# Optimization experiments

Hardware: AMD Instinct MI355X
Metric: run time of the kernel (lower is better)

Reference implementation:

```python
import jax, jax.numpy as jnp
import numpy as np

B, C, H, HEADS, WS, TOPK = 16, 112, 64, 4, 4, 128
NWH = H // WS          # 16 windows per side
NWIN = NWH * NWH       # 256 windows
HD = C // HEADS        # 28
SCALE = HD ** -0.5


def _topk_indices():
    # Geometric top-K closest full-res pixels per window center (level 0 of focal attention).
    f = H // NWH  # window stride on full-res grid
    qh = np.arange(NWH) * f + f // 2
    cq = np.stack(np.meshgrid(qh, qh, indexing='ij'), 0).reshape(2, -1)            # (2, NWIN)
    ck = np.stack(np.meshgrid(np.arange(H), np.arange(H), indexing='ij'), 0).reshape(2, -1)  # (2, H*H)
    d = np.sqrt(((cq[:, :, None].astype(np.float32) - ck[:, None, :]) ** 2).sum(0))
    return np.argsort(d, axis=1, kind='stable')[:, :TOPK].astype(np.int32)        # (NWIN, TOPK)


def setup_inputs() -> dict:
    key = jax.random.key(0)
    k1, k2, k3 = jax.random.split(key, 3)
    return {
        'x': jax.random.normal(k1, (B, C, H, H), jnp.float32),
        'Wqkv': jax.random.normal(k2, (3 * C, C), jnp.float32) * 0.02,
        'Wproj': jax.random.normal(k3, (C, C), jnp.float32) * 0.02,
        'bproj': jnp.zeros((C,), jnp.float32),
        'topk_idx': jnp.asarray(_topk_indices()),
    }


def reference(x, Wqkv, Wproj, bproj, topk_idx):
    Bv, Cv, Hv, Wv = x.shape
    nwin = (Hv // WS) * (Wv // WS)
    xt = jnp.transpose(x, (0, 2, 3, 1))                       # (B, H, W, C)
    qkv = jnp.einsum('bhwc,dc->bhwd', xt, Wqkv)               # 1x1 conv == matmul
    q, k, v = jnp.split(qkv, 3, axis=-1)
    # Window-partition queries: (B*nwin, heads, ws^2, hd)
    qw = q.reshape(Bv, Hv // WS, WS, Wv // WS, WS, Cv)
    qw = jnp.transpose(qw, (0, 1, 3, 2, 4, 5)).reshape(Bv * nwin, WS * WS, HEADS, HD)
    qw = jnp.transpose(qw, (0, 2, 1, 3)) * SCALE
    # Gather top-K K/V tokens per window from the full-resolution token list
    kf = k.reshape(Bv, Hv * Wv, HEADS, HD)
    vf = v.reshape(Bv, Hv * Wv, HEADS, HD)
    ksel = kf[:, topk_idx]                                    # (B, nwin, TOPK, heads, hd)
    vsel = vf[:, topk_idx]
    ksel = jnp.transpose(ksel, (0, 1, 3, 2, 4)).reshape(Bv * nwin, HEADS, TOPK, HD)
    vsel = jnp.transpose(vsel, (0, 1, 3, 2, 4)).reshape(Bv * nwin, HEADS, TOPK, HD)
    # Windowed attention over gathered KV
    attn = jax.nn.softmax(jnp.einsum('whqd,whkd->whqk', qw, ksel), axis=-1)
    o = jnp.einsum('whqk,whkd->whqd', attn, vsel)             # (B*nwin, heads, ws^2, hd)
    o = jnp.transpose(o, (0, 2, 1, 3)).reshape(Bv * nwin, WS * WS, Cv)
    # Window reverse -> (B, H, W, C)
    o = o.reshape(Bv, Hv // WS, Wv // WS, WS, WS, Cv)
    o = jnp.transpose(o, (0, 1, 3, 2, 4, 5)).reshape(Bv, Hv, Wv, Cv)
    out = jnp.einsum('bhwc,dc->bhwd', o, Wproj) + bproj
    return jnp.transpose(out, (0, 3, 1, 2))                   # (B, C, H, W)
```

## Files before the change

### kernel.cpp

```cpp
#include <hip/hip_runtime.h>
#include <hip/hip_bf16.h>
#include <cstdint>

#define B_ 16
#define C_ 112
#define HEADS_ 4
#define HD_ 28
#define NWIN_ 256
#define TOPK_ 128
#define D3_ 336
#define SCALE_ 0.18898223650461363f

typedef __attribute__((ext_vector_type(4))) float f32x4;
typedef __attribute__((ext_vector_type(8))) short short8;
typedef unsigned uint4u __attribute__((ext_vector_type(4), aligned(4)));

union Frag { unsigned u[4]; uint4 u4; short8 s; };

__device__ inline unsigned cvtpk(float a, float b) {
    unsigned r;
    asm("v_cvt_pk_bf16_f32 %0, %1, %2" : "=v"(r) : "v"(a), "v"(b));
    return r;
}
__device__ inline float bflo(unsigned u) { return __uint_as_float(u << 16); }
__device__ inline float bfhi(unsigned u) { return __uint_as_float(u & 0xFFFF0000u); }

__global__ __launch_bounds__(256) void wt_kernel(const float* __restrict__ W, const float* __restrict__ Wp,
                                                 uint4* __restrict__ WAq,
                                                 uint4* __restrict__ WAh, uint4* __restrict__ WAl) {
    const int id = blockIdx.x * 256 + threadIdx.x;
    if (id < 5376) {
        const int ks = id / 1344, rem = id % 1344;
        const int tile = rem >> 6, l = rem & 63;
        const int d = tile * 16 + (l & 15);
        const int cb = ks * 32 + (l >> 4) * 8;
        float v[8];
        #pragma unroll
        for (int j = 0; j < 8; ++j) { int c = cb + j; v[j] = (c < C_) ? W[d * C_ + c] : 0.f; }
        uint4 o;
        o.x = cvtpk(v[0], v[1]); o.y = cvtpk(v[2], v[3]);
        o.z = cvtpk(v[4], v[5]); o.w = cvtpk(v[6], v[7]);
        WAq[id] = o;
    } else if (id < 5376 + 1792) {
        const int id2 = id - 5376;
        const int ks = id2 / 448, rem = id2 % 448;
        const int tile = rem >> 6, l = rem & 63;
        const int d = tile * 16 + (l & 15);
        const int cb = ks * 32 + (l >> 4) * 8;
        float v[8];
        #pragma unroll
        for (int j = 0; j < 8; ++j) { int c = cb + j; v[j] = (c < C_) ? Wp[d * C_ + c] : 0.f; }
        unsigned hw_[4], lw_[4];
        #pragma unroll
        for (int p = 0; p < 4; ++p) {
            unsigned hh = cvtpk(v[2 * p], v[2 * p + 1]);
            hw_[p] = hh;
            lw_[p] = cvtpk(v[2 * p] - bflo(hh), v[2 * p + 1] - bfhi(hh));
        }
        WAh[id2] = make_uint4(hw_[0], hw_[1], hw_[2], hw_[3]);
        WAl[id2] = make_uint4(lw_[0], lw_[1], lw_[2], lw_[3]);
    }
}

__global__ __launch_bounds__(256) void qkv_kernel(const float* __restrict__ x,
                                                  const uint4* __restrict__ WAq,
                                                  ushort* __restrict__ qkv) {
    __shared__ unsigned xs[64][132];
    const int hw0 = blockIdx.x << 7;
    const int dblk = blockIdx.y;
    const int b = blockIdx.z;
    const int tid = threadIdx.x;
    for (int i = tid; i < 2048; i += 256) {
        const int c2 = i >> 5, j4 = (i & 31) << 2;
        uint4 o = make_uint4(0, 0, 0, 0);
        if (c2 < 56) {
            const float* r0 = x + (((size_t)b * C_ + 2 * c2) << 12) + hw0 + j4;
            float4 a = *(const float4*)r0;
            float4 c = *(const float4*)(r0 + 4096);
            o.x = cvtpk(a.x, c.x); o.y = cvtpk(a.y, c.y);
            o.z = cvtpk(a.z, c.z); o.w = cvtpk(a.w, c.w);
        }
        *(uint4*)&xs[c2][j4] = o;
    }
    __syncthreads();
    const int wv = tid >> 6, l = tid & 63, lq = l & 15, g = l >> 4;
    const int hwl = wv << 5;
    f32x4 acc[7][2] = {};
    #pragma unroll
    for (int ks = 0; ks < 4; ++ks) {
        Frag bf[2];
        #pragma unroll
        for (int n = 0; n < 2; ++n) {
            const int col = hwl + (n << 4) + lq;
            const int r0 = (ks << 4) + (g << 2);
            bf[n].u[0] = xs[r0][col]; bf[n].u[1] = xs[r0 + 1][col];
            bf[n].u[2] = xs[r0 + 2][col]; bf[n].u[3] = xs[r0 + 3][col];
        }
        const uint4* wp = WAq + ((ks * 21 + dblk * 7) << 6) + l;
        #pragma unroll
        for (int m = 0; m < 7; ++m) {
            Frag af; af.u4 = wp[m << 6];
            acc[m][0] = __builtin_amdgcn_mfma_f32_16x16x32_bf16(af.s, bf[0].s, acc[m][0], 0, 0, 0);
            acc[m][1] = __builtin_amdgcn_mfma_f32_16x16x32_bf16(af.s, bf[1].s, acc[m][1], 0, 0, 0);
        }
    }
    const size_t hwbase = ((size_t)b << 12) + hw0;
    #pragma unroll
    for (int m = 0; m < 7; ++m) {
        const int d0 = dblk * 112 + (m << 4) + (g << 2);
        #pragma unroll
        for (int n = 0; n < 2; ++n) {
            const int hw = hwl + (n << 4) + lq;
            uint2 o2;
            o2.x = cvtpk(acc[m][n][0], acc[m][n][1]);
            o2.y = cvtpk(acc[m][n][2], acc[m][n][3]);
            *(uint2*)(qkv + (hwbase + hw) * D3_ + d0) = o2;
        }
    }
}

__global__ __launch_bounds__(256) void attn_kernel(const ushort* __restrict__ qkv,
                                                   const int* __restrict__ topk,
                                                   const uint4* __restrict__ WAh,
                                                   const uint4* __restrict__ WAl,
                                                   const float* __restrict__ bp,
                                                   float* __restrict__ out) {
    __shared__ int idxs[TOPK_];
    __shared__ __align__(16) unsigned vsT[4][32][68];
    __shared__ __align__(16) unsigned plds[4][16][68];
    const int b = blockIdx.y, w = blockIdx.x;
    const int wy = w >> 4, wx = w & 15;
    const int tid = threadIdx.x;
    const int wv = tid >> 6, l = tid & 63, lq = l & 15, g = l >> 4;
    if (tid < TOPK_) idxs[tid] = topk[w * TOPK_ + tid];
    __syncthreads();
    const int h = wv;
    const size_t bbase = (size_t)(b << 12);
    const int hwq = ((wy * 4 + (lq >> 2)) << 6) + (wx << 2) + (lq & 3);
    Frag qf;
    {
        uint4u t = *(const uint4u*)(qkv + (bbase + hwq) * D3_ + h * HD_ + (g << 3));
        qf.u[0] = t[0]; qf.u[1] = t[1];
        qf.u[2] = (g == 3) ? 0u : t[2];
        qf.u[3] = (g == 3) ? 0u : t[3];
    }
    Frag kf[8];
    #pragma unroll
    for (int m = 0; m < 8; ++m) {
        const int kr = idxs[(m << 4) + lq];
        uint4u t = *(const uint4u*)(qkv + (bbase + kr) * D3_ + C_ + h * HD_ + (g << 3));
        kf[m].u[0] = t[0]; kf[m].u[1] = t[1]; kf[m].u[2] = t[2]; kf[m].u[3] = t[3];
    }
    {
        const ushort* v0 = qkv + (bbase + idxs[2 * l]) * D3_ + 2 * C_ + h * HD_;
        const ushort* v1 = qkv + (bbase + idxs[2 * l + 1]) * D3_ + 2 * C_ + h * HD_;
        unsigned w0[14], w1[14];
        { uint4u a = *(const uint4u*)v0;        w0[0]=a[0]; w0[1]=a[1]; w0[2]=a[2]; w0[3]=a[3]; }
        { uint4u a = *(const uint4u*)(v0 + 8);  w0[4]=a[0]; w0[5]=a[1]; w0[6]=a[2]; w0[7]=a[3]; }
        { uint4u a = *(const uint4u*)(v0 + 16); w0[8]=a[0]; w0[9]=a[1]; w0[10]=a[2]; w0[11]=a[3]; }
        { uint2 a = *(const uint2*)(v0 + 24);   w0[12]=a.x; w0[13]=a.y; }
        { uint4u a = *(const uint4u*)v1;        w1[0]=a[0]; w1[1]=a[1]; w1[2]=a[2]; w1[3]=a[3]; }
        { uint4u a = *(const uint4u*)(v1 + 8);  w1[4]=a[0]; w1[5]=a[1]; w1[6]=a[2]; w1[7]=a[3]; }
        { uint4u a = *(const uint4u*)(v1 + 16); w1[8]=a[0]; w1[9]=a[1]; w1[10]=a[2]; w1[11]=a[3]; }
        { uint2 a = *(const uint2*)(v1 + 24);   w1[12]=a.x; w1[13]=a.y; }
        #pragma unroll
        for (int j = 0; j < 14; ++j) {
            vsT[wv][2 * j][l]     = __builtin_amdgcn_perm(w1[j], w0[j], 0x05040100);
            vsT[wv][2 * j + 1][l] = __builtin_amdgcn_perm(w1[j], w0[j], 0x07060302);
        }
    }
    f32x4 sacc[8];
    #pragma unroll
    for (int m = 0; m < 8; ++m) {
        f32x4 z = {0.f, 0.f, 0.f, 0.f};
        sacc[m] = __builtin_amdgcn_mfma_f32_16x16x32_bf16(kf[m].s, qf.s, z, 0, 0, 0);
    }
    float mx = -1e30f;
    #pragma unroll
    for (int m = 0; m < 8; ++m)
        #pragma unroll
        for (int r = 0; r < 4; ++r) { sacc[m][r] *= SCALE_; mx = fmaxf(mx, sacc[m][r]); }
    mx = fmaxf(mx, __shfl_xor(mx, 16, 64));
    mx = fmaxf(mx, __shfl_xor(mx, 32, 64));
    float sum = 0.f;
    #pragma unroll
    for (int m = 0; m < 8; ++m)
        #pragma unroll
        for (int r = 0; r < 4; ++r) { float e = __expf(sacc[m][r] - mx); sacc[m][r] = e; sum += e; }
    sum += __shfl_xor(sum, 16, 64);
    sum += __shfl_xor(sum, 32, 64);
    const float inv = 1.f / sum;
    #pragma unroll
    for (int m = 0; m < 8; ++m) {
        unsigned u0 = cvtpk(sacc[m][0] * inv, sacc[m][1] * inv);
        unsigned u1 = cvtpk(sacc[m][2] * inv, sacc[m][3] * inv);
        *(uint2*)&plds[wv][lq][(m << 3) + (g << 1)] = make_uint2(u0, u1);
    }
    f32x4 oacc[2] = {};
    #pragma unroll
    for (int ks = 0; ks < 4; ++ks) {
        Frag pb;
        pb.u4 = *(const uint4*)&plds[wv][lq][(g << 2) + (ks << 4)];
        #pragma unroll
        for (int m = 0; m < 2; ++m) {
            Frag va;
            va.u4 = *(const uint4*)&vsT[wv][lq + (m << 4)][(g << 2) + (ks << 4)];
            oacc[m] = __builtin_amdgcn_mfma_f32_16x16x32_bf16(va.s, pb.s, oacc[m], 0, 0, 0);
        }
    }
    __syncthreads();
    float* os = (float*)&plds[0][0][0];
    for (int i = 1904 + tid; i < 2176; i += 256) os[i] = 0.f;
    #pragma unroll
    for (int m = 0; m < 2; ++m) {
        const int d0 = (g << 2) + (m << 4);
        if (d0 < HD_) {
            #pragma unroll
            for (int r = 0; r < 4; ++r)
                os[(h * HD_ + d0 + r) * 17 + lq] = oacc[m][r];
        }
    }
    __syncthreads();
    f32x4 pacc[2] = {};
    #pragma unroll
    for (int ks = 0; ks < 4; ++ks) {
        const int cb = (g << 3) + (ks << 5);
        float v[8];
        #pragma unroll
        for (int j = 0; j < 8; ++j) v[j] = os[(cb + j) * 17 + lq];
        Frag bh, bl;
        #pragma unroll
        for (int p = 0; p < 4; ++p) {
            unsigned hh = cvtpk(v[2 * p], v[2 * p + 1]);
            bh.u[p] = hh;
            bl.u[p] = cvtpk(v[2 * p] - bflo(hh), v[2 * p + 1] - bfhi(hh));
        }
        #pragma unroll
        for (int mi = 0; mi < 2; ++mi) {
            const int m = (wv << 1) + mi;
            if (m < 7) {
                Frag ah, al;
                ah.u4 = WAh[((ks * 7 + m) << 6) + l];
                al.u4 = WAl[((ks * 7 + m) << 6) + l];
                pacc[mi] = __builtin_amdgcn_mfma_f32_16x16x32_bf16(ah.s, bh.s, pacc[mi], 0, 0, 0);
                pacc[mi] = __builtin_amdgcn_mfma_f32_16x16x32_bf16(ah.s, bl.s, pacc[mi], 0, 0, 0);
                pacc[mi] = __builtin_amdgcn_mfma_f32_16x16x32_bf16(al.s, bh.s, pacc[mi], 0, 0, 0);
            }
        }
    }
    #pragma unroll
    for (int mi = 0; mi < 2; ++mi) {
        const int m = (wv << 1) + mi;
        if (m < 7) {
            const int d0 = (m << 4) + (g << 2);
            const float4 bias = *(const float4*)(bp + d0);
            out[(((size_t)(b * C_ + d0 + 0)) << 12) + hwq] = pacc[mi][0] + bias.x;
            out[(((size_t)(b * C_ + d0 + 1)) << 12) + hwq] = pacc[mi][1] + bias.y;
            out[(((size_t)(b * C_ + d0 + 2)) << 12) + hwq] = pacc[mi][2] + bias.z;
            out[(((size_t)(b * C_ + d0 + 3)) << 12) + hwq] = pacc[mi][3] + bias.w;
        }
    }
}

extern "C" void kernel_launch(void* const* d_in, const int* in_sizes, int n_in,
                              void* d_out, int out_size, void* d_ws, size_t ws_size,
                              hipStream_t stream) {
    const float* x     = (const float*)d_in[0];
    const float* Wqkv  = (const float*)d_in[1];
    const float* Wproj = (const float*)d_in[2];
    const float* bproj = (const float*)d_in[3];
    const int*   topk  = (const int*)d_in[4];
    float* out = (float*)d_out;
    char* ws = (char*)d_ws;
    ushort* qkv = (ushort*)ws;
    uint4*  WAq = (uint4*)(ws + 44040192);
    uint4*  WAh = (uint4*)(ws + 44040192 + 86016);
    uint4*  WAl = (uint4*)(ws + 44040192 + 86016 + 28672);
    wt_kernel<<<28, 256, 0, stream>>>(Wqkv, Wproj, WAq, WAh, WAl);
    qkv_kernel<<<dim3(32, 3, 16), 256, 0, stream>>>(x, WAq, qkv);
    attn_kernel<<<dim3(NWIN_, 16), 256, 0, stream>>>(qkv, topk, WAh, WAl, bproj, out);
}
```

Before: 155.6 us.

## Compute all QKV blocks per workgroup, remap attn blocks per XCD, prefetch proj weights

The QKV kernel now loads and converts each x tile into shared memory once and loops over all three output-channel blocks, instead of launching three workgroups that each reload the same tile. The attention kernel flattens its grid and remaps block IDs so that each XCD gets a contiguous range of windows, aiming for better L2 locality on the gathered K/V rows. It also loads the projection weight fragments early, before the V transpose, so their latency overlaps other work. The cost is fewer QKV workgroups (512) and higher register pressure in both kernels.

```diff
diff --git a/kernel.cpp b/kernel.cpp
--- a/kernel.cpp
+++ b/kernel.cpp
@@ -67,8 +67,7 @@
                                                   ushort* __restrict__ qkv) {
     __shared__ unsigned xs[64][132];
     const int hw0 = blockIdx.x << 7;
-    const int dblk = blockIdx.y;
-    const int b = blockIdx.z;
+    const int b = blockIdx.y;
     const int tid = threadIdx.x;
     for (int i = tid; i < 2048; i += 256) {
         const int c2 = i >> 5, j4 = (i & 31) << 2;
@@ -85,36 +84,41 @@
     __syncthreads();
     const int wv = tid >> 6, l = tid & 63, lq = l & 15, g = l >> 4;
     const int hwl = wv << 5;
-    f32x4 acc[7][2] = {};
-    #pragma unroll
-    for (int ks = 0; ks < 4; ++ks) {
-        Frag bf[2];
+    Frag bf[4][2];
+    #pragma unroll
+    for (int ks = 0; ks < 4; ++ks)
         #pragma unroll
         for (int n = 0; n < 2; ++n) {
             const int col = hwl + (n << 4) + lq;
             const int r0 = (ks << 4) + (g << 2);
-            bf[n].u[0] = xs[r0][col]; bf[n].u[1] = xs[r0 + 1][col];
-            bf[n].u[2] = xs[r0 + 2][col]; bf[n].u[3] = xs[r0 + 3][col];
-        }
-        const uint4* wp = WAq + ((ks * 21 + dblk * 7) << 6) + l;
+            bf[ks][n].u[0] = xs[r0][col]; bf[ks][n].u[1] = xs[r0 + 1][col];
+            bf[ks][n].u[2] = xs[r0 + 2][col]; bf[ks][n].u[3] = xs[r0 + 3][col];
+        }
+    const size_t hwbase = ((size_t)b << 12) + hw0;
+    #pragma unroll
+    for (int dblk = 0; dblk < 3; ++dblk) {
+        f32x4 acc[7][2] = {};
+        #pragma unroll
+        for (int ks = 0; ks < 4; ++ks) {
+            const uint4* wp = WAq + ((ks * 21 + dblk * 7) << 6) + l;
+            #pragma unroll
+            for (int m = 0; m < 7; ++m) {
+                Frag af; af.u4 = wp[m << 6];
+                acc[m][0] = __builtin_amdgcn_mfma_f32_16x16x32_bf16(af.s, bf[ks][0].s, acc[m][0], 0, 0, 0);
+                acc[m][1] = __builtin_amdgcn_mfma_f32_16x16x32_bf16(af.s, bf[ks][1].s, acc[m][1], 0, 0, 0);
+            }
+        }
         #pragma unroll
         for (int m = 0; m < 7; ++m) {
-            Frag af; af.u4 = wp[m << 6];
-            acc[m][0] = __builtin_amdgcn_mfma_f32_16x16x32_bf16(af.s, bf[0].s, acc[m][0], 0, 0, 0);
-            acc[m][1] = __builtin_amdgcn_mfma_f32_16x16x32_bf16(af.s, bf[1].s, acc[m][1], 0, 0, 0);
-        }
-    }
-    const size_t hwbase = ((size_t)b << 12) + hw0;
-    #pragma unroll
-    for (int m = 0; m < 7; ++m) {
-        const int d0 = dblk * 112 + (m << 4) + (g << 2);
-        #pragma unroll
-        for (int n = 0; n < 2; ++n) {
-            const int hw = hwl + (n << 4) + lq;
-            uint2 o2;
-            o2.x = cvtpk(acc[m][n][0], acc[m][n][1]);
-            o2.y = cvtpk(acc[m][n][2], acc[m][n][3]);
-            *(uint2*)(qkv + (hwbase + hw) * D3_ + d0) = o2;
+            const int d0 = dblk * 112 + (m << 4) + (g << 2);
+            #pragma unroll
+            for (int n = 0; n < 2; ++n) {
+                const int hw = hwl + (n << 4) + lq;
+                uint2 o2;
+                o2.x = cvtpk(acc[m][n][0], acc[m][n][1]);
+                o2.y = cvtpk(acc[m][n][2], acc[m][n][3]);
+                *(uint2*)(qkv + (hwbase + hw) * D3_ + d0) = o2;
+            }
         }
     }
 }
@@ -128,7 +132,10 @@
     __shared__ int idxs[TOPK_];
     __shared__ __align__(16) unsigned vsT[4][32][68];
     __shared__ __align__(16) unsigned plds[4][16][68];
-    const int b = blockIdx.y, w = blockIdx.x;
+    const int bid = blockIdx.x;
+    const int xcd = bid & 7, j = bid >> 3;
+    const int b = j >> 5;
+    const int w = (xcd << 5) | (j & 31);
     const int wy = w >> 4, wx = w & 15;
     const int tid = threadIdx.x;
     const int wv = tid >> 6, l = tid & 63, lq = l & 15, g = l >> 4;
@@ -150,6 +157,21 @@
         const int kr = idxs[(m << 4) + lq];
         uint4u t = *(const uint4u*)(qkv + (bbase + kr) * D3_ + C_ + h * HD_ + (g << 3));
         kf[m].u[0] = t[0]; kf[m].u[1] = t[1]; kf[m].u[2] = t[2]; kf[m].u[3] = t[3];
+    }
+    Frag wah[2][4], wal[2][4];
+    #pragma unroll
+    for (int mi = 0; mi < 2; ++mi) {
+        const int m = (wv << 1) + mi;
+        #pragma unroll
+        for (int ks = 0; ks < 4; ++ks) {
+            if (m < 7) {
+                wah[mi][ks].u4 = WAh[((ks * 7 + m) << 6) + l];
+                wal[mi][ks].u4 = WAl[((ks * 7 + m) << 6) + l];
+            } else {
+                wah[mi][ks].u4 = make_uint4(0, 0, 0, 0);
+                wal[mi][ks].u4 = make_uint4(0, 0, 0, 0);
+            }
+        }
     }
     {
         const ushort* v0 = qkv + (bbase + idxs[2 * l]) * D3_ + 2 * C_ + h * HD_;
@@ -164,9 +186,9 @@
         { uint4u a = *(const uint4u*)(v1 + 16); w1[8]=a[0]; w1[9]=a[1]; w1[10]=a[2]; w1[11]=a[3]; }
         { uint2 a = *(const uint2*)(v1 + 24);   w1[12]=a.x; w1[13]=a.y; }
         #pragma unroll
-        for (int j = 0; j < 14; ++j) {
-            vsT[wv][2 * j][l]     = __builtin_amdgcn_perm(w1[j], w0[j], 0x05040100);
-            vsT[wv][2 * j + 1][l] = __builtin_amdgcn_perm(w1[j], w0[j], 0x07060302);
+        for (int jj = 0; jj < 14; ++jj) {
+            vsT[wv][2 * jj][l]     = __builtin_amdgcn_perm(w1[jj], w0[jj], 0x05040100);
+            vsT[wv][2 * jj + 1][l] = __builtin_amdgcn_perm(w1[jj], w0[jj], 0x07060302);
         }
     }
     f32x4 sacc[8];
@@ -227,7 +249,7 @@
         const int cb = (g << 3) + (ks << 5);
         float v[8];
         #pragma unroll
-        for (int j = 0; j < 8; ++j) v[j] = os[(cb + j) * 17 + lq];
+        for (int jj = 0; jj < 8; ++jj) v[jj] = os[(cb + jj) * 17 + lq];
         Frag bh, bl;
         #pragma unroll
         for (int p = 0; p < 4; ++p) {
@@ -237,15 +259,9 @@
         }
         #pragma unroll
         for (int mi = 0; mi < 2; ++mi) {
-            const int m = (wv << 1) + mi;
-            if (m < 7) {
-                Frag ah, al;
-                ah.u4 = WAh[((ks * 7 + m) << 6) + l];
-                al.u4 = WAl[((ks * 7 + m) << 6) + l];
-                pacc[mi] = __builtin_amdgcn_mfma_f32_16x16x32_bf16(ah.s, bh.s, pacc[mi], 0, 0, 0);
-                pacc[mi] = __builtin_amdgcn_mfma_f32_16x16x32_bf16(ah.s, bl.s, pacc[mi], 0, 0, 0);
-                pacc[mi] = __builtin_amdgcn_mfma_f32_16x16x32_bf16(al.s, bh.s, pacc[mi], 0, 0, 0);
-            }
+            pacc[mi] = __builtin_amdgcn_mfma_f32_16x16x32_bf16(wah[mi][ks].s, bh.s, pacc[mi], 0, 0, 0);
+            pacc[mi] = __builtin_amdgcn_mfma_f32_16x16x32_bf16(wah[mi][ks].s, bl.s, pacc[mi], 0, 0, 0);
+            pacc[mi] = __builtin_amdgcn_mfma_f32_16x16x32_bf16(wal[mi][ks].s, bh.s, pacc[mi], 0, 0, 0);
         }
     }
     #pragma unroll
@@ -277,6 +293,6 @@
     uint4*  WAh = (uint4*)(ws + 44040192 + 86016);
     uint4*  WAl = (uint4*)(ws + 44040192 + 86016 + 28672);
     wt_kernel<<<28, 256, 0, stream>>>(Wqkv, Wproj, WAq, WAh, WAl);
-    qkv_kernel<<<dim3(32, 3, 16), 256, 0, stream>>>(x, WAq, qkv);
-    attn_kernel<<<dim3(NWIN_, 16), 256, 0, stream>>>(qkv, topk, WAh, WAl, bproj, out);
-}
+    qkv_kernel<<<dim3(32, 16), 256, 0, stream>>>(x, WAq, qkv);
+    attn_kernel<<<dim3(NWIN_ * B_), 256, 0, stream>>>(qkv, topk, WAh, WAl, bproj, out);
+}
```

Result: slower. 160.7 us (+3.3%).
